# Optimization experiments

Hardware: AMD Instinct MI355X
Metric: run time of the kernel (lower is better)

Reference implementation:

```python
import jax, jax.numpy as jnp
import numpy as np

B, N, C = 4, 2048, 1024
H = 16
D = C // H  # head_dim = 64
SCALE = D ** -0.5


def setup_inputs() -> dict:
    key = jax.random.key(0)
    ks = jax.random.split(key, 5)
    s = 0.02
    return {
        "x": jax.random.normal(ks[0], (B, N, C), dtype=jnp.float32),
        "wq": jax.random.normal(ks[1], (C, C), dtype=jnp.float32) * s,
        "wk": jax.random.normal(ks[2], (C, C), dtype=jnp.float32) * s,
        "wv": jax.random.normal(ks[3], (C, C), dtype=jnp.float32) * s,
        "wo": jax.random.normal(ks[4], (C, C), dtype=jnp.float32) * s,
        "bo": jnp.zeros((C,), dtype=jnp.float32),
    }


def reference(x, wq, wk, wv, wo, bo):
    # nn.Linear: y = x @ W^T (no bias for q/k/v since qkv_bias=False)
    b, n, c = x.shape
    q = (x @ wq.T).reshape(b, n, H, D).transpose(0, 2, 1, 3)  # [B,H,N,D]
    k = (x @ wk.T).reshape(b, n, H, D).transpose(0, 2, 1, 3)
    v = (x @ wv.T).reshape(b, n, H, D).transpose(0, 2, 1, 3)
    q = q * SCALE
    attn = jax.nn.softmax(jnp.einsum("bhnd,bhmd->bhnm", q, k), axis=-1)
    out = jnp.einsum("bhnm,bhmd->bhnd", attn, v)  # [B,H,N,D]
    out = out.transpose(0, 2, 1, 3).reshape(b, n, c)
    return out @ wo.T + bo
```

## Files before the change

### kernel.cpp

```cpp
#include <hip/hip_runtime.h>
#include <hip/hip_bf16.h>
#include <stdint.h>


#define GAS __attribute__((address_space(1)))
#define LAS __attribute__((address_space(3)))

typedef __attribute__((ext_vector_type(8))) short v8s;
typedef __attribute__((ext_vector_type(4))) float v4f;

__device__ __forceinline__ unsigned short f2bf(float f) {
  __hip_bfloat16 h = __float2bfloat16(f);
  return __builtin_bit_cast(unsigned short, h);
}

__device__ __forceinline__ float fexp2(float x) {
#if __has_builtin(__builtin_amdgcn_exp2f)
  return __builtin_amdgcn_exp2f(x);
#else
  return __expf(x * 0.6931471805599453f);
#endif
}

__device__ __forceinline__ void gld_lds16(const void* g, void* l) {
  __builtin_amdgcn_global_load_lds((GAS void*)(uintptr_t)g,
                                   (LAS void*)(uint32_t)(uintptr_t)l,
                                   16, 0, 0);
}

__global__ void cvt_f32_bf16(const float* __restrict__ src,
                             unsigned short* __restrict__ dst, int n4) {
  int i = blockIdx.x * blockDim.x + threadIdx.x;
  const int stride = gridDim.x * blockDim.x;
  for (; i < n4; i += stride) {
    float4 f = ((const float4*)src)[i];
    ushort4 u;
    u.x = f2bf(f.x); u.y = f2bf(f.y); u.z = f2bf(f.z); u.w = f2bf(f.w);
    ((ushort4*)dst)[i] = u;
  }
}

template<int OUTMODE>
__global__ __launch_bounds__(256)
void gemm_bt(const unsigned short* __restrict__ A,
             const unsigned short* __restrict__ Bm,
             void* __restrict__ Cout, const float* __restrict__ bias,
             int M, int N, int K, int scaleCols, float scaleVal)
{
  __shared__ unsigned short sA[128 * 64];
  __shared__ unsigned short sB[128 * 64];

  const int tid  = threadIdx.x;
  const int lane = tid & 63;
  const int w    = tid >> 6;
  const int g    = lane >> 4;
  const int r16  = lane & 15;
  const long bm  = (long)blockIdx.y * 128;
  const long bn  = (long)blockIdx.x * 128;
  const int  wm  = (w >> 1) * 64;
  const int  wn  = (w & 1) * 64;

  v4f acc[4][4] = {};

  for (int k0 = 0; k0 < K; k0 += 64) {
    #pragma unroll
    for (int t4 = 0; t4 < 4; ++t4) {
      const int t   = t4 * 4 + w;
      const int row = t * 8 + (lane >> 3);
      const long co = (long)k0 + (lane & 7) * 8;
      gld_lds16(A  + (bm + row) * K + co, (char*)sA + t * 1024);
      gld_lds16(Bm + (bn + row) * K + co, (char*)sB + t * 1024);
    }
    __syncthreads();

    v8s af[4][2], bf[4][2];
    #pragma unroll
    for (int m = 0; m < 4; ++m)
      #pragma unroll
      for (int kk = 0; kk < 2; ++kk)
        af[m][kk] = *(const v8s*)(sA + (wm + m*16 + r16)*64 + kk*32 + g*8);
    #pragma unroll
    for (int n = 0; n < 4; ++n)
      #pragma unroll
      for (int kk = 0; kk < 2; ++kk)
        bf[n][kk] = *(const v8s*)(sB + (wn + n*16 + r16)*64 + kk*32 + g*8);
    #pragma unroll
    for (int kk = 0; kk < 2; ++kk)
      #pragma unroll
      for (int m = 0; m < 4; ++m)
        #pragma unroll
        for (int n = 0; n < 4; ++n)
          acc[m][n] = __builtin_amdgcn_mfma_f32_16x16x32_bf16(
              af[m][kk], bf[n][kk], acc[m][n], 0, 0, 0);
    __syncthreads();
  }

  #pragma unroll
  for (int m = 0; m < 4; ++m) {
    #pragma unroll
    for (int n = 0; n < 4; ++n) {
      const long row0 = bm + wm + m*16 + g*4;
      const long col  = bn + wn + n*16 + r16;
      if constexpr (OUTMODE == 0) {
        unsigned short* Cb = (unsigned short*)Cout;
        const float sc = (col < scaleCols) ? scaleVal : 1.0f;
        #pragma unroll
        for (int r = 0; r < 4; ++r)
          Cb[(row0 + r) * N + col] = f2bf(acc[m][n][r] * sc);
      } else {
        float* Cf = (float*)Cout;
        const float bv = bias[col];
        #pragma unroll
        for (int r = 0; r < 4; ++r)
          Cf[(row0 + r) * N + col] = acc[m][n][r] + bv;
      }
    }
  }
}

__global__ __launch_bounds__(256)
void attn_fwd(const unsigned short* __restrict__ Qkv,
              unsigned short* __restrict__ O)
{
  __shared__ unsigned short sK[128 * 64];
  __shared__ unsigned int   sVT32[64 * 64];
  __shared__ unsigned short sP[4][16 * 128];

  const unsigned short* sVTe = (const unsigned short*)sVT32;
  const int tid  = threadIdx.x;
  const int lane = tid & 63;
  const int w    = tid >> 6;
  const int g    = lane >> 4;
  const int r16  = lane & 15;
  const int b  = blockIdx.z;
  const int h  = blockIdx.y;
  const int qb = blockIdx.x;
  const long kvbase = (long)b * 2048;
  const long qrow0w = kvbase + qb * 64 + w * 16;
  const int ld = 3072;

  v8s qf[2];
  #pragma unroll
  for (int kk = 0; kk < 2; ++kk)
    qf[kk] = *(const v8s*)(Qkv + (qrow0w + r16) * ld + h*64 + kk*32 + g*8);

  v4f oacc[4] = {};
  float mrow[4], lsum[4];
  #pragma unroll
  for (int r = 0; r < 4; ++r) { mrow[r] = -__builtin_inff(); lsum[r] = 0.0f; }

  for (int kv0 = 0; kv0 < 2048; kv0 += 128) {
    #pragma unroll
    for (int t4 = 0; t4 < 4; ++t4) {
      const int t    = t4 * 4 + w;
      const int row  = t * 8 + (lane >> 3);
      const int csrc = (lane & 7) ^ ((lane >> 3) & 7);
      gld_lds16(Qkv + (kvbase + kv0 + row) * ld + 1024 + h*64 + csrc*8,
                (char*)sK + t * 1024);
    }
    {
      const int jp = lane;
      const int d0 = w * 16;
      const unsigned short* vs = Qkv + (kvbase + kv0 + 2*jp) * ld + 2048 + h*64 + d0;
      v8s va0 = *(const v8s*)vs;
      v8s va1 = *(const v8s*)(vs + 8);
      v8s vb0 = *(const v8s*)(vs + ld);
      v8s vb1 = *(const v8s*)(vs + ld + 8);
      #pragma unroll
      for (int e = 0; e < 8; ++e) {
        int d = d0 + e;
        sVT32[d*64 + (((jp >> 2) ^ (d & 15)) << 2) + (jp & 3)] =
            ((unsigned)(unsigned short)vb0[e] << 16) | (unsigned short)va0[e];
        d = d0 + 8 + e;
        sVT32[d*64 + (((jp >> 2) ^ (d & 15)) << 2) + (jp & 3)] =
            ((unsigned)(unsigned short)vb1[e] << 16) | (unsigned short)va1[e];
      }
    }
    __syncthreads();

    v4f sacc[8] = {};
    #pragma unroll
    for (int n = 0; n < 8; ++n) {
      const int row = n*16 + r16;
      v8s k0 = *(const v8s*)(sK + row*64 + (((0*4+g) ^ (row & 7)) << 3));
      v8s k1 = *(const v8s*)(sK + row*64 + (((1*4+g) ^ (row & 7)) << 3));
      sacc[n] = __builtin_amdgcn_mfma_f32_16x16x32_bf16(qf[0], k0, sacc[n], 0, 0, 0);
      sacc[n] = __builtin_amdgcn_mfma_f32_16x16x32_bf16(qf[1], k1, sacc[n], 0, 0, 0);
    }

    float mx[4];
    #pragma unroll
    for (int r = 0; r < 4; ++r) {
      float v = fmaxf(fmaxf(fmaxf(sacc[0][r], sacc[1][r]),
                            fmaxf(sacc[2][r], sacc[3][r])),
                      fmaxf(fmaxf(sacc[4][r], sacc[5][r]),
                            fmaxf(sacc[6][r], sacc[7][r])));
      v = fmaxf(v, __shfl_xor(v, 1));
      v = fmaxf(v, __shfl_xor(v, 2));
      v = fmaxf(v, __shfl_xor(v, 4));
      v = fmaxf(v, __shfl_xor(v, 8));
      mx[r] = v;
    }
    const float need = fmaxf(fmaxf(mx[0] - mrow[0], mx[1] - mrow[1]),
                             fmaxf(mx[2] - mrow[2], mx[3] - mrow[3]));
    if (__any(need > 8.0f)) {
      #pragma unroll
      for (int r = 0; r < 4; ++r) {
        const float mnew  = fmaxf(mrow[r], mx[r]);
        const float alpha = fexp2(mrow[r] - mnew);
        mrow[r] = mnew;
        lsum[r] *= alpha;
        #pragma unroll
        for (int n = 0; n < 4; ++n) oacc[n][r] *= alpha;
      }
    }
    #pragma unroll
    for (int n = 0; n < 8; ++n)
      #pragma unroll
      for (int r = 0; r < 4; ++r) {
        const float p = fexp2(sacc[n][r] - mrow[r]);
        sacc[n][r] = p;
        lsum[r] += p;
      }

    unsigned short* pb = &sP[w][0];
    #pragma unroll
    for (int n = 0; n < 8; ++n) {
      const int col = n*16 + r16;
      const int ch  = col >> 3;
      #pragma unroll
      for (int r = 0; r < 4; ++r) {
        const int row = g*4 + r;
        pb[row*128 + ((ch ^ row) << 3) + (col & 7)] = f2bf(sacc[n][r]);
      }
    }

    #pragma unroll
    for (int kk = 0; kk < 4; ++kk) {
      v8s pf = *(const v8s*)(pb + r16*128 + (((kk*4+g) ^ r16) << 3));
      #pragma unroll
      for (int n = 0; n < 4; ++n) {
        const int d = n*16 + r16;
        v8s vf = *(const v8s*)(sVTe + d*128 + (((kk*4+g) ^ (d & 15)) << 3));
        oacc[n] = __builtin_amdgcn_mfma_f32_16x16x32_bf16(pf, vf, oacc[n], 0, 0, 0);
      }
    }
    __syncthreads();
  }

  float rs[4];
  #pragma unroll
  for (int r = 0; r < 4; ++r) {
    float s = lsum[r];
    s += __shfl_xor(s, 1);
    s += __shfl_xor(s, 2);
    s += __shfl_xor(s, 4);
    s += __shfl_xor(s, 8);
    rs[r] = 1.0f / s;
  }
  #pragma unroll
  for (int n = 0; n < 4; ++n) {
    const int col = h*64 + n*16 + r16;
    #pragma unroll
    for (int r = 0; r < 4; ++r)
      O[(qrow0w + g*4 + r) * 1024 + col] = f2bf(oacc[n][r] * rs[r]);
  }
}

extern "C" void kernel_launch(void* const* d_in, const int* in_sizes, int n_in,
                              void* d_out, int out_size, void* d_ws, size_t ws_size,
                              hipStream_t stream)
{
  const float* x  = (const float*)d_in[0];
  const float* wq = (const float*)d_in[1];
  const float* wk = (const float*)d_in[2];
  const float* wv = (const float*)d_in[3];
  const float* wo = (const float*)d_in[4];
  const float* bo = (const float*)d_in[5];

  unsigned short* Xb   = (unsigned short*)d_ws;
  unsigned short* Wqkv = Xb   + (size_t)8192 * 1024;
  unsigned short* Wob  = Wqkv + (size_t)3072 * 1024;
  unsigned short* Qkv  = Wob  + (size_t)1024 * 1024;
  unsigned short* Obuf = Xb;
  float* out = (float*)d_out;

  cvt_f32_bf16<<<2048, 256, 0, stream>>>(x,  Xb,   8192 * 1024 / 4);
  cvt_f32_bf16<<<512,  256, 0, stream>>>(wq, Wqkv,              1024 * 1024 / 4);
  cvt_f32_bf16<<<512,  256, 0, stream>>>(wk, Wqkv + 1024*1024,  1024 * 1024 / 4);
  cvt_f32_bf16<<<512,  256, 0, stream>>>(wv, Wqkv + 2*1024*1024,1024 * 1024 / 4);
  cvt_f32_bf16<<<512,  256, 0, stream>>>(wo, Wob,               1024 * 1024 / 4);

  gemm_bt<0><<<dim3(24, 64), 256, 0, stream>>>(Xb, Wqkv, Qkv, nullptr,
                                               8192, 3072, 1024, 1024,
                                               0.18033688011112042f);
  attn_fwd<<<dim3(32, 16, 4), 256, 0, stream>>>(Qkv, Obuf);
  gemm_bt<1><<<dim3(8, 64), 256, 0, stream>>>(Obuf, Wob, out, bo,
                                              8192, 1024, 1024, 0, 1.0f);
}
```

Baseline: 385.9 us.

## Double-buffer K/V tiles in attention to overlap loads with compute

The attention kernel now keeps two LDS buffers for K and transposed V. It prefetches the next KV tile, with K going straight to LDS and V going into registers, while the current tile is being computed. The trailing per-iteration barrier is removed and s_setprio is raised around the MFMA sections. This aims to hide global load latency behind compute, at the cost of doubled LDS use, which may reduce occupancy, and more register pressure from holding V in registers.

Result: no change. 383.7 us (-0.6%).

```diff
diff --git a/kernel.cpp b/kernel.cpp
--- a/kernel.cpp
+++ b/kernel.cpp
@@ -122,11 +122,10 @@
 void attn_fwd(const unsigned short* __restrict__ Qkv,
               unsigned short* __restrict__ O)
 {
-  __shared__ unsigned short sK[128 * 64];
-  __shared__ unsigned int   sVT32[64 * 64];
+  __shared__ unsigned short sK[2][128 * 64];
+  __shared__ unsigned int   sVT32[2][64 * 64];
   __shared__ unsigned short sP[4][16 * 128];
 
-  const unsigned short* sVTe = (const unsigned short*)sVT32;
   const int tid  = threadIdx.x;
   const int lane = tid & 63;
   const int w    = tid >> 6;
@@ -139,6 +138,12 @@
   const long qrow0w = kvbase + qb * 64 + w * 16;
   const int ld = 3072;
 
+  const int  rowk = w * 8 + (lane >> 3);
+  const int  csrc = (lane & 7) ^ ((lane >> 3) & 7);
+  const unsigned short* Kb = Qkv + 1024 + h*64 + csrc*8;
+  const int  jp = lane, d0v = w * 16;
+  const unsigned short* Vb = Qkv + 2048 + h*64 + d0v;
+
   v8s qf[2];
   #pragma unroll
   for (int kk = 0; kk < 2; ++kk)
@@ -149,44 +154,60 @@
   #pragma unroll
   for (int r = 0; r < 4; ++r) { mrow[r] = -__builtin_inff(); lsum[r] = 0.0f; }
 
-  for (int kv0 = 0; kv0 < 2048; kv0 += 128) {
-    #pragma unroll
-    for (int t4 = 0; t4 < 4; ++t4) {
-      const int t    = t4 * 4 + w;
-      const int row  = t * 8 + (lane >> 3);
-      const int csrc = (lane & 7) ^ ((lane >> 3) & 7);
-      gld_lds16(Qkv + (kvbase + kv0 + row) * ld + 1024 + h*64 + csrc*8,
-                (char*)sK + t * 1024);
-    }
-    {
-      const int jp = lane;
-      const int d0 = w * 16;
-      const unsigned short* vs = Qkv + (kvbase + kv0 + 2*jp) * ld + 2048 + h*64 + d0;
-      v8s va0 = *(const v8s*)vs;
-      v8s va1 = *(const v8s*)(vs + 8);
-      v8s vb0 = *(const v8s*)(vs + ld);
-      v8s vb1 = *(const v8s*)(vs + ld + 8);
-      #pragma unroll
-      for (int e = 0; e < 8; ++e) {
-        int d = d0 + e;
-        sVT32[d*64 + (((jp >> 2) ^ (d & 15)) << 2) + (jp & 3)] =
-            ((unsigned)(unsigned short)vb0[e] << 16) | (unsigned short)va0[e];
-        d = d0 + 8 + e;
-        sVT32[d*64 + (((jp >> 2) ^ (d & 15)) << 2) + (jp & 3)] =
-            ((unsigned)(unsigned short)vb1[e] << 16) | (unsigned short)va1[e];
-      }
+  v8s vreg[4];
+  #pragma unroll
+  for (int t4 = 0; t4 < 4; ++t4)
+    gld_lds16(Kb + (kvbase + t4*32 + rowk) * ld,
+              (char*)sK[0] + (t4*4 + w) * 1024);
+  {
+    const unsigned short* vs = Vb + (kvbase + 2*jp) * ld;
+    vreg[0] = *(const v8s*)vs;
+    vreg[1] = *(const v8s*)(vs + 8);
+    vreg[2] = *(const v8s*)(vs + ld);
+    vreg[3] = *(const v8s*)(vs + ld + 8);
+  }
+
+  for (int t = 0; t < 16; ++t) {
+    unsigned short* sKc  = &sK[t & 1][0];
+    unsigned int*   sVTc = &sVT32[t & 1][0];
+    const unsigned short* sVTe = (const unsigned short*)sVTc;
+
+    asm volatile("s_waitcnt vmcnt(0)" ::: "memory");
+    #pragma unroll
+    for (int e = 0; e < 8; ++e) {
+      int d = d0v + e;
+      sVTc[d*64 + (((jp >> 2) ^ (d & 15)) << 2) + (jp & 3)] =
+          ((unsigned)(unsigned short)vreg[2][e] << 16) | (unsigned short)vreg[0][e];
+      d = d0v + 8 + e;
+      sVTc[d*64 + (((jp >> 2) ^ (d & 15)) << 2) + (jp & 3)] =
+          ((unsigned)(unsigned short)vreg[3][e] << 16) | (unsigned short)vreg[1][e];
     }
     __syncthreads();
 
+    if (t < 15) {
+      const long kvn = kvbase + (long)(t + 1) * 128;
+      char* sKn = (char*)&sK[(t + 1) & 1][0];
+      #pragma unroll
+      for (int t4 = 0; t4 < 4; ++t4)
+        gld_lds16(Kb + (kvn + t4*32 + rowk) * ld, sKn + (t4*4 + w) * 1024);
+      const unsigned short* vs = Vb + (kvn + 2*jp) * ld;
+      vreg[0] = *(const v8s*)vs;
+      vreg[1] = *(const v8s*)(vs + 8);
+      vreg[2] = *(const v8s*)(vs + ld);
+      vreg[3] = *(const v8s*)(vs + ld + 8);
+    }
+
     v4f sacc[8] = {};
+    __builtin_amdgcn_s_setprio(1);
     #pragma unroll
     for (int n = 0; n < 8; ++n) {
       const int row = n*16 + r16;
-      v8s k0 = *(const v8s*)(sK + row*64 + (((0*4+g) ^ (row & 7)) << 3));
-      v8s k1 = *(const v8s*)(sK + row*64 + (((1*4+g) ^ (row & 7)) << 3));
+      v8s k0 = *(const v8s*)(sKc + row*64 + ((g ^ (row & 7)) << 3));
+      v8s k1 = *(const v8s*)(sKc + row*64 + (((4 + g) ^ (row & 7)) << 3));
       sacc[n] = __builtin_amdgcn_mfma_f32_16x16x32_bf16(qf[0], k0, sacc[n], 0, 0, 0);
       sacc[n] = __builtin_amdgcn_mfma_f32_16x16x32_bf16(qf[1], k1, sacc[n], 0, 0, 0);
     }
+    __builtin_amdgcn_s_setprio(0);
 
     float mx[4];
     #pragma unroll
@@ -235,17 +256,18 @@
       }
     }
 
+    __builtin_amdgcn_s_setprio(1);
     #pragma unroll
     for (int kk = 0; kk < 4; ++kk) {
-      v8s pf = *(const v8s*)(pb + r16*128 + (((kk*4+g) ^ r16) << 3));
+      v8s pf = *(const v8s*)(pb + r16*128 + (((kk*4 + g) ^ r16) << 3));
       #pragma unroll
       for (int n = 0; n < 4; ++n) {
         const int d = n*16 + r16;
-        v8s vf = *(const v8s*)(sVTe + d*128 + (((kk*4+g) ^ (d & 15)) << 3));
+        v8s vf = *(const v8s*)(sVTe + d*128 + (((kk*4 + g) ^ (d & 15)) << 3));
         oacc[n] = __builtin_amdgcn_mfma_f32_16x16x32_bf16(pf, vf, oacc[n], 0, 0, 0);
       }
     }
-    __syncthreads();
+    __builtin_amdgcn_s_setprio(0);
   }
 
   float rs[4];
```
